# Performance work log

Hardware: AMD Instinct MI355X
Metric: run time of the kernel (lower is better)

The kernel has to match this reference:

```python
import jax, jax.numpy as jnp
import numpy as np

N_NODES = 100000
N_EDGES = 1600000
D_FEAT = 64


def setup_inputs() -> dict:
    key = jax.random.key(0)
    k1, k2, k3, k4 = jax.random.split(key, 4)
    rows = jax.random.randint(k1, (N_EDGES,), 0, N_NODES, dtype=jnp.int32)
    cols = jax.random.randint(k2, (N_EDGES,), 0, N_NODES, dtype=jnp.int32)
    vals = jax.random.uniform(k3, (N_EDGES,), dtype=jnp.float32)
    embeds = jax.random.normal(k4, (N_NODES, D_FEAT), dtype=jnp.float32)
    return {"rows": rows, "cols": cols, "vals": vals, "embeds": embeds,
            "n_nodes": N_NODES}


def reference(rows, cols, vals, embeds, n_nodes):
    # GCN sparse aggregation: res[i] = sum_{e: rows[e]==i} vals[e] * embeds[cols[e]]
    # Equivalent to adj.matmul(embeds) with adj in COO form.
    msgs = vals[:, None] * embeds[cols]            # [E, D] gather + scale
    res = jax.ops.segment_sum(msgs, rows, num_segments=n_nodes)  # [N, D] scatter-add
    return res
```

## Files before the change

kernel.cpp:

```cpp
#include <hip/hip_runtime.h>
#include <hip/hip_bf16.h>


#define D_FEAT 64
#define LOG_RPB 7
#define ROWS_PER_BUCKET 128
#define N_BUCKETS 782
#define PB 512
#define K1_CAP 3136
#define K4_CAP 3072

typedef unsigned long long u64;

__global__ __launch_bounds__(256) void gcn_scatter_fallback(
    const int* __restrict__ rows, const int* __restrict__ cols,
    const float* __restrict__ vals, const float* __restrict__ embeds,
    float* __restrict__ out, int n_edges)
{
    int gtid = blockIdx.x * blockDim.x + threadIdx.x;
    int e = gtid >> 4;
    if (e >= n_edges) return;
    int lane4 = gtid & 15;
    int row = rows[e]; int col = cols[e]; float v = vals[e];
    const float4* ep = reinterpret_cast<const float4*>(embeds + (size_t)col * D_FEAT);
    float4 m = ep[lane4];
    float* op = out + (size_t)row * D_FEAT + lane4 * 4;
    atomicAdd(op + 0, v * m.x);
    atomicAdd(op + 1, v * m.y);
    atomicAdd(op + 2, v * m.z);
    atomicAdd(op + 3, v * m.w);
}

__device__ inline int wave_incl_scan(int x, int lane) {
    #pragma unroll
    for (int o = 1; o < 64; o <<= 1) {
        int y = __shfl_up(x, o, 64);
        if (lane >= o) x += y;
    }
    return x;
}

__global__ __launch_bounds__(1024, 8) void k_partition_conv(
    const int* __restrict__ rows, const int* __restrict__ cols,
    const float* __restrict__ vals, u64* __restrict__ sorted,
    int* __restrict__ offg, const float* __restrict__ embeds,
    unsigned short* __restrict__ emb16, int do_conv,
    int n_edges, int n_elems, int chunk)
{
    __shared__ u64 ebuf[K1_CAP];
    __shared__ int lh[N_BUCKETS];
    __shared__ int cur[N_BUCKETS];
    __shared__ int segtot[16];

    int blk = blockIdx.x, tid = threadIdx.x;
    int lane = tid & 63, wid = tid >> 6;
    int beg = blk * chunk;
    int end = min(beg + chunk, n_edges);
    int cnt = end - beg;

    for (int i = tid; i < N_BUCKETS; i += 1024) lh[i] = 0;
    __syncthreads();
    for (int e = beg + tid; e < end; e += 1024)
        atomicAdd(&lh[rows[e] >> LOG_RPB], 1);
    __syncthreads();

    for (int seg = wid; seg * 64 < N_BUCKETS; seg += 16) {
        int idx = seg * 64 + lane;
        int v = (idx < N_BUCKETS) ? lh[idx] : 0;
        int inc = wave_incl_scan(v, lane);
        if (idx < N_BUCKETS) lh[idx] = inc - v;
        if (lane == 63) segtot[seg] = inc;
    }
    __syncthreads();
    if (tid < 64) {
        int v = (tid < 13) ? segtot[tid] : 0;
        int inc = wave_incl_scan(v, tid);
        if (tid < 13) segtot[tid] = inc - v;
    }
    __syncthreads();
    int* myoff = offg + (size_t)blk * (N_BUCKETS + 1);
    for (int i = tid; i < N_BUCKETS; i += 1024) {
        int excl = lh[i] + segtot[i >> 6];
        myoff[i] = excl;
        cur[i] = excl;
    }
    if (tid == 0) myoff[N_BUCKETS] = cnt;
    __syncthreads();

    for (int e = beg + tid; e < end; e += 1024) {
        int r = rows[e];
        int b = r >> LOG_RPB;
        unsigned meta = (unsigned)cols[e] |
                        ((unsigned)(r & (ROWS_PER_BUCKET - 1)) << 17);
        u64 ent = ((u64)__float_as_uint(vals[e]) << 32) | meta;
        int p = atomicAdd(&cur[b], 1);
        ebuf[p] = ent;
    }
    __syncthreads();

    for (int i = tid; i < cnt; i += 1024)
        sorted[beg + i] = ebuf[i];

    if (do_conv) {
        for (int i = blk * 1024 + tid; i < n_elems; i += PB * 1024) {
            unsigned u = __float_as_uint(embeds[i]);
            unsigned r = (u + 0x7FFFu + ((u >> 16) & 1u)) >> 16;
            emb16[i] = (unsigned short)r;
        }
    }
}

template <bool USE16>
__global__ __launch_bounds__(512) void k_aggregate_seg(
    const u64* __restrict__ sorted, const int* __restrict__ offg,
    const float* __restrict__ embeds, const unsigned short* __restrict__ emb16,
    float* __restrict__ out, int n_nodes, int chunk)
{
    __shared__ u64 ebuf[K4_CAP];
    __shared__ int sOff[PB], sLen[PB], sBase[PB];
    __shared__ int wtot[8];
    __shared__ int rcnt[ROWS_PER_BUCKET];
    __shared__ int roff[ROWS_PER_BUCKET + 1];
    __shared__ int rcur[ROWS_PER_BUCKET];

    int b = blockIdx.x, tid = threadIdx.x;
    int lane = tid & 63, wid = tid >> 6;
    int rowbase = b * ROWS_PER_BUCKET;
    int nrows = n_nodes - rowbase;
    if (nrows > ROWS_PER_BUCKET) nrows = ROWS_PER_BUCKET;

    if (tid < PB) {
        int o0 = offg[(size_t)tid * (N_BUCKETS + 1) + b];
        int o1 = offg[(size_t)tid * (N_BUCKETS + 1) + b + 1];
        sOff[tid] = o0;
        sLen[tid] = o1 - o0;
    }
    for (int i = tid; i < ROWS_PER_BUCKET; i += 512) rcnt[i] = 0;
    __syncthreads();

    {
        int v = sLen[wid * 64 + lane];
        int inc = wave_incl_scan(v, lane);
        sBase[wid * 64 + lane] = inc - v;
        if (lane == 63) wtot[wid] = inc;
    }
    __syncthreads();
    {
        int c = 0;
        for (int w = 0; w < wid; ++w) c += wtot[w];
        sBase[wid * 64 + lane] += c;
    }
    int n = 0;
    for (int w = 0; w < 8; ++w) n += wtot[w];
    __syncthreads();

    if (n <= K4_CAP) {
        for (int g = wid; g < PB / 16; g += 8) {
            int seg = g * 16 + (lane >> 2);
            int len = sLen[seg];
            const u64* sp = sorted + (size_t)seg * chunk + sOff[seg];
            for (int i = (lane & 3); i < len; i += 4)
                atomicAdd(&rcnt[(int)((sp[i] >> 17) & (ROWS_PER_BUCKET - 1))], 1);
        }
        __syncthreads();

        if (tid < 64) {
            int a = rcnt[tid], c = rcnt[64 + tid];
            int ia = wave_incl_scan(a, tid);
            int ta = __shfl(ia, 63, 64);
            int ic = wave_incl_scan(c, tid);
            int ea = ia - a;
            int ec = ta + ic - c;
            roff[tid] = ea;       rcur[tid] = ea;
            roff[64 + tid] = ec;  rcur[64 + tid] = ec;
            if (tid == 63) roff[ROWS_PER_BUCKET] = ta + __shfl(ic, 63, 64);
        }
        __syncthreads();

        for (int g = wid; g < PB / 16; g += 8) {
            int seg = g * 16 + (lane >> 2);
            int len = sLen[seg];
            const u64* sp = sorted + (size_t)seg * chunk + sOff[seg];
            for (int i = (lane & 3); i < len; i += 4) {
                u64 ent = sp[i];
                int lr = (int)((ent >> 17) & (ROWS_PER_BUCKET - 1));
                int p = atomicAdd(&rcur[lr], 1);
                ebuf[p] = ent;
            }
        }
        __syncthreads();

        for (int lr = wid; lr < ROWS_PER_BUCKET; lr += 8) {
            int rs = roff[lr], re = roff[lr + 1];
            float acc = 0.0f;
            int j = rs;
            #define GATHER(t) (USE16 \
                ? __uint_as_float((unsigned)emb16[(size_t)((t) & 0x1FFFF) * D_FEAT + lane] << 16) \
                : embeds[(size_t)((t) & 0x1FFFF) * D_FEAT + lane])
            for (; j + 7 < re; j += 8) {
                u64 t0 = ebuf[j + 0], t1 = ebuf[j + 1], t2 = ebuf[j + 2], t3 = ebuf[j + 3];
                u64 t4 = ebuf[j + 4], t5 = ebuf[j + 5], t6 = ebuf[j + 6], t7 = ebuf[j + 7];
                float m0 = GATHER(t0), m1 = GATHER(t1), m2 = GATHER(t2), m3 = GATHER(t3);
                float m4 = GATHER(t4), m5 = GATHER(t5), m6 = GATHER(t6), m7 = GATHER(t7);
                acc += __uint_as_float((unsigned)(t0 >> 32)) * m0;
                acc += __uint_as_float((unsigned)(t1 >> 32)) * m1;
                acc += __uint_as_float((unsigned)(t2 >> 32)) * m2;
                acc += __uint_as_float((unsigned)(t3 >> 32)) * m3;
                acc += __uint_as_float((unsigned)(t4 >> 32)) * m4;
                acc += __uint_as_float((unsigned)(t5 >> 32)) * m5;
                acc += __uint_as_float((unsigned)(t6 >> 32)) * m6;
                acc += __uint_as_float((unsigned)(t7 >> 32)) * m7;
            }
            for (; j + 3 < re; j += 4) {
                u64 t0 = ebuf[j + 0], t1 = ebuf[j + 1], t2 = ebuf[j + 2], t3 = ebuf[j + 3];
                float m0 = GATHER(t0), m1 = GATHER(t1), m2 = GATHER(t2), m3 = GATHER(t3);
                acc += __uint_as_float((unsigned)(t0 >> 32)) * m0;
                acc += __uint_as_float((unsigned)(t1 >> 32)) * m1;
                acc += __uint_as_float((unsigned)(t2 >> 32)) * m2;
                acc += __uint_as_float((unsigned)(t3 >> 32)) * m3;
            }
            for (; j < re; ++j) {
                u64 t0 = ebuf[j];
                acc += __uint_as_float((unsigned)(t0 >> 32)) * GATHER(t0);
            }
            #undef GATHER
            if (lr < nrows)
                out[(size_t)(rowbase + lr) * D_FEAT + lane] = acc;
        }
    } else {
        for (int i = tid; i < nrows * D_FEAT; i += 512)
            out[(size_t)rowbase * D_FEAT + i] = 0.0f;
        __syncthreads();
        for (int seg = wid; seg < PB; seg += 8) {
            int len = sLen[seg];
            const u64* sp = sorted + (size_t)seg * chunk + sOff[seg];
            for (int i = 0; i < len; ++i) {
                u64 ent = sp[i];
                int lr = (int)((ent >> 17) & (ROWS_PER_BUCKET - 1));
                int c = (int)(ent & 0x1FFFF);
                float v = __uint_as_float((unsigned)(ent >> 32));
                float m = embeds[(size_t)c * D_FEAT + lane];
                atomicAdd(&out[(size_t)(rowbase + lr) * D_FEAT + lane], v * m);
            }
        }
    }
}

extern "C" void kernel_launch(void* const* d_in, const int* in_sizes, int n_in,
                              void* d_out, int out_size, void* d_ws, size_t ws_size,
                              hipStream_t stream) {
    const int*   rows   = (const int*)d_in[0];
    const int*   cols   = (const int*)d_in[1];
    const float* vals   = (const float*)d_in[2];
    const float* embeds = (const float*)d_in[3];

    float* out = (float*)d_out;
    int n_edges = in_sizes[0];
    int n_nodes = out_size / D_FEAT;
    int n_buckets = (n_nodes + ROWS_PER_BUCKET - 1) >> LOG_RPB;
    int chunk = (n_edges + PB - 1) / PB;
    int n_elems = n_nodes * D_FEAT;

    size_t base_need = (size_t)n_edges * sizeof(u64) +
                       (size_t)PB * (N_BUCKETS + 1) * sizeof(int) + 256;
    size_t full_need = base_need + (size_t)n_elems * sizeof(unsigned short) + 256;

    if (n_buckets != N_BUCKETS || chunk > K1_CAP || ws_size < base_need) {
        hipMemsetAsync(out, 0, (size_t)out_size * sizeof(float), stream);
        long long total_threads = (long long)n_edges * 16;
        int block = 256;
        int grid = (int)((total_threads + block - 1) / block);
        gcn_scatter_fallback<<<grid, block, 0, stream>>>(rows, cols, vals, embeds, out, n_edges);
        return;
    }

    u64* sorted = (u64*)d_ws;
    int* offg   = (int*)(sorted + n_edges);
    unsigned short* emb16 = (unsigned short*)
        (((uintptr_t)(offg + (size_t)PB * (N_BUCKETS + 1)) + 15) & ~(uintptr_t)15);

    bool use16 = (ws_size >= full_need);

    k_partition_conv<<<PB, 1024, 0, stream>>>(rows, cols, vals, sorted, offg,
                                              embeds, emb16, use16 ? 1 : 0,
                                              n_edges, n_elems, chunk);
    if (use16)
        k_aggregate_seg<true><<<N_BUCKETS, 512, 0, stream>>>(
            sorted, offg, embeds, emb16, out, n_nodes, chunk);
    else
        k_aggregate_seg<false><<<N_BUCKETS, 512, 0, stream>>>(
            sorted, offg, embeds, emb16, out, n_nodes, chunk);
}
```

Baseline: 152.5 us.

## Fuse partition and aggregation into one cooperative kernel with a work queue

Merges the bucket-partition and per-bucket aggregation kernels into one cooperative launch of 512 blocks of 1024 threads, separated by grid.sync. After the sync, blocks pull buckets from a global atomic work queue. Edges are now loaded once into registers and reused for both the histogram and scatter passes, and the bf16 conversion is vectorised to float4. A global-atomic fallback is added for buckets whose edges exceed shared-memory capacity. The cooperative launch needs all 512 blocks to be co-resident, and the larger shared footprint plus 1024-thread blocks in the aggregation phase may lower occupancy and latency hiding for the gathers.

```diff
diff --git a/kernel.cpp b/kernel.cpp
--- a/kernel.cpp
+++ b/kernel.cpp
@@ -1,5 +1,8 @@
 #include <hip/hip_runtime.h>
 #include <hip/hip_bf16.h>
+#include <hip/hip_cooperative_groups.h>
+
+namespace cg = cooperative_groups;
 
 
 #define D_FEAT 64
@@ -8,9 +11,22 @@
 #define N_BUCKETS 782
 #define PB 512
 #define K1_CAP 3136
-#define K4_CAP 3072
 
 typedef unsigned long long u64;
+
+__device__ inline unsigned bf16rne(float x) {
+    unsigned u = __float_as_uint(x);
+    return (u + 0x7FFFu + ((u >> 16) & 1u)) >> 16;
+}
+
+__device__ inline int wave_incl_scan(int x, int lane) {
+    #pragma unroll
+    for (int o = 1; o < 64; o <<= 1) {
+        int y = __shfl_up(x, o, 64);
+        if (lane >= o) x += y;
+    }
+    return x;
+}
 
 __global__ __launch_bounds__(256) void gcn_scatter_fallback(
     const int* __restrict__ rows, const int* __restrict__ cols,
@@ -31,13 +47,231 @@
     atomicAdd(op + 3, v * m.w);
 }
 
-__device__ inline int wave_incl_scan(int x, int lane) {
-    #pragma unroll
-    for (int o = 1; o < 64; o <<= 1) {
-        int y = __shfl_up(x, o, 64);
-        if (lane >= o) x += y;
-    }
-    return x;
+template <bool USE16>
+__global__ __launch_bounds__(1024, 8) void k_fused(
+    const int* __restrict__ rows, const int* __restrict__ cols,
+    const float* __restrict__ vals, const float* __restrict__ embeds,
+    unsigned short* __restrict__ emb16, u64* __restrict__ sorted,
+    int* __restrict__ offg, int* __restrict__ wq, float* __restrict__ out,
+    int n_edges, int n_nodes, int n_elems, int chunk)
+{
+    __shared__ u64 ebuf[K1_CAP];
+    __shared__ int lh[N_BUCKETS];
+    __shared__ int cur[N_BUCKETS];
+    __shared__ int segtot[16];
+    __shared__ int sOff[PB], sLen[PB];
+    __shared__ int wtot[16];
+    __shared__ int rcnt[ROWS_PER_BUCKET];
+    __shared__ int roff[ROWS_PER_BUCKET + 1];
+    __shared__ int rcur[ROWS_PER_BUCKET];
+    __shared__ int sbucket;
+
+    cg::grid_group grid = cg::this_grid();
+
+    int blk = blockIdx.x, tid = threadIdx.x;
+    int lane = tid & 63, wid = tid >> 6;
+
+    {
+        int beg = blk * chunk;
+        int end = min(beg + chunk, n_edges);
+        int cnt = end - beg;
+
+        for (int i = tid; i < N_BUCKETS; i += 1024) lh[i] = 0;
+        __syncthreads();
+
+        u64 ent[4]; int eb[4]; bool okk[4];
+        #pragma unroll
+        for (int k = 0; k < 4; ++k) {
+            int e = beg + k * 1024 + tid;
+            okk[k] = (e < end);
+            if (okk[k]) {
+                int r = rows[e];
+                eb[k] = r >> LOG_RPB;
+                unsigned meta = (unsigned)cols[e] |
+                                ((unsigned)(r & (ROWS_PER_BUCKET - 1)) << 17);
+                ent[k] = ((u64)__float_as_uint(vals[e]) << 32) | meta;
+                atomicAdd(&lh[eb[k]], 1);
+            }
+        }
+        __syncthreads();
+
+        for (int seg = wid; seg * 64 < N_BUCKETS; seg += 16) {
+            int idx = seg * 64 + lane;
+            int v = (idx < N_BUCKETS) ? lh[idx] : 0;
+            int inc = wave_incl_scan(v, lane);
+            if (idx < N_BUCKETS) lh[idx] = inc - v;
+            if (lane == 63) segtot[seg] = inc;
+        }
+        __syncthreads();
+        if (tid < 64) {
+            int v = (tid < 13) ? segtot[tid] : 0;
+            int inc = wave_incl_scan(v, tid);
+            if (tid < 13) segtot[tid] = inc - v;
+        }
+        __syncthreads();
+        int* myoff = offg + (size_t)blk * (N_BUCKETS + 1);
+        for (int i = tid; i < N_BUCKETS; i += 1024) {
+            int excl = lh[i] + segtot[i >> 6];
+            myoff[i] = excl;
+            cur[i] = excl;
+        }
+        if (tid == 0) myoff[N_BUCKETS] = cnt;
+        __syncthreads();
+
+        #pragma unroll
+        for (int k = 0; k < 4; ++k) {
+            if (okk[k]) {
+                int p = atomicAdd(&cur[eb[k]], 1);
+                ebuf[p] = ent[k];
+            }
+        }
+        __syncthreads();
+
+        for (int i = tid; i < cnt; i += 1024)
+            sorted[beg + i] = ebuf[i];
+
+        if (USE16) {
+            const float4* src4 = (const float4*)embeds;
+            u64* dst4 = (u64*)emb16;
+            int nq = n_elems >> 2;
+            for (int i = blk * 1024 + tid; i < nq; i += PB * 1024) {
+                float4 f = src4[i];
+                u64 pk = (u64)bf16rne(f.x) | ((u64)bf16rne(f.y) << 16) |
+                         ((u64)bf16rne(f.z) << 32) | ((u64)bf16rne(f.w) << 48);
+                dst4[i] = pk;
+            }
+            if (blk == 0 && tid < (n_elems & 3)) {
+                int i = (nq << 2) + tid;
+                emb16[i] = (unsigned short)bf16rne(embeds[i]);
+            }
+        }
+        if (blk == 0 && tid == 0) *wq = 0;
+    }
+
+    grid.sync();
+
+    for (;;) {
+        __syncthreads();
+        if (tid == 0) sbucket = atomicAdd(wq, 1);
+        __syncthreads();
+        int b = sbucket;
+        if (b >= N_BUCKETS) break;
+
+        int rowbase = b * ROWS_PER_BUCKET;
+        int nrows = n_nodes - rowbase;
+        if (nrows > ROWS_PER_BUCKET) nrows = ROWS_PER_BUCKET;
+
+        if (tid < PB) {
+            int o0 = offg[(size_t)tid * (N_BUCKETS + 1) + b];
+            int o1 = offg[(size_t)tid * (N_BUCKETS + 1) + b + 1];
+            sOff[tid] = o0;
+            sLen[tid] = o1 - o0;
+        }
+        for (int i = tid; i < ROWS_PER_BUCKET; i += 1024) rcnt[i] = 0;
+        __syncthreads();
+
+        if (wid < 8) {
+            int v = sLen[wid * 64 + lane];
+            #pragma unroll
+            for (int o = 32; o > 0; o >>= 1) v += __shfl_down(v, o, 64);
+            if (lane == 0) wtot[wid] = v;
+        }
+        __syncthreads();
+        int n = 0;
+        #pragma unroll
+        for (int w = 0; w < 8; ++w) n += wtot[w];
+
+        if (n <= K1_CAP) {
+            {
+                int seg = tid >> 1;
+                int len = sLen[seg];
+                const u64* sp = sorted + (size_t)seg * chunk + sOff[seg];
+                for (int i = (tid & 1); i < len; i += 2)
+                    atomicAdd(&rcnt[(int)((sp[i] >> 17) & (ROWS_PER_BUCKET - 1))], 1);
+            }
+            __syncthreads();
+
+            if (tid < 64) {
+                int a = rcnt[tid], c = rcnt[64 + tid];
+                int ia = wave_incl_scan(a, tid);
+                int ta = __shfl(ia, 63, 64);
+                int ic = wave_incl_scan(c, tid);
+                int ea = ia - a;
+                int ec = ta + ic - c;
+                roff[tid] = ea;       rcur[tid] = ea;
+                roff[64 + tid] = ec;  rcur[64 + tid] = ec;
+                if (tid == 63) roff[ROWS_PER_BUCKET] = ta + __shfl(ic, 63, 64);
+            }
+            __syncthreads();
+
+            {
+                int seg = tid >> 1;
+                int len = sLen[seg];
+                const u64* sp = sorted + (size_t)seg * chunk + sOff[seg];
+                for (int i = (tid & 1); i < len; i += 2) {
+                    u64 ent = sp[i];
+                    int lr = (int)((ent >> 17) & (ROWS_PER_BUCKET - 1));
+                    int p = atomicAdd(&rcur[lr], 1);
+                    ebuf[p] = ent;
+                }
+            }
+            __syncthreads();
+
+            for (int lr = wid; lr < ROWS_PER_BUCKET; lr += 16) {
+                int rs = roff[lr], re = roff[lr + 1];
+                float acc = 0.0f;
+                int j = rs;
+                #define GATHER(t) (USE16 \
+                    ? __uint_as_float((unsigned)emb16[(size_t)((t) & 0x1FFFF) * D_FEAT + lane] << 16) \
+                    : embeds[(size_t)((t) & 0x1FFFF) * D_FEAT + lane])
+                for (; j + 7 < re; j += 8) {
+                    u64 t0 = ebuf[j + 0], t1 = ebuf[j + 1], t2 = ebuf[j + 2], t3 = ebuf[j + 3];
+                    u64 t4 = ebuf[j + 4], t5 = ebuf[j + 5], t6 = ebuf[j + 6], t7 = ebuf[j + 7];
+                    float m0 = GATHER(t0), m1 = GATHER(t1), m2 = GATHER(t2), m3 = GATHER(t3);
+                    float m4 = GATHER(t4), m5 = GATHER(t5), m6 = GATHER(t6), m7 = GATHER(t7);
+                    acc += __uint_as_float((unsigned)(t0 >> 32)) * m0;
+                    acc += __uint_as_float((unsigned)(t1 >> 32)) * m1;
+                    acc += __uint_as_float((unsigned)(t2 >> 32)) * m2;
+                    acc += __uint_as_float((unsigned)(t3 >> 32)) * m3;
+                    acc += __uint_as_float((unsigned)(t4 >> 32)) * m4;
+                    acc += __uint_as_float((unsigned)(t5 >> 32)) * m5;
+                    acc += __uint_as_float((unsigned)(t6 >> 32)) * m6;
+                    acc += __uint_as_float((unsigned)(t7 >> 32)) * m7;
+                }
+                for (; j + 3 < re; j += 4) {
+                    u64 t0 = ebuf[j + 0], t1 = ebuf[j + 1], t2 = ebuf[j + 2], t3 = ebuf[j + 3];
+                    float m0 = GATHER(t0), m1 = GATHER(t1), m2 = GATHER(t2), m3 = GATHER(t3);
+                    acc += __uint_as_float((unsigned)(t0 >> 32)) * m0;
+                    acc += __uint_as_float((unsigned)(t1 >> 32)) * m1;
+                    acc += __uint_as_float((unsigned)(t2 >> 32)) * m2;
+                    acc += __uint_as_float((unsigned)(t3 >> 32)) * m3;
+                }
+                for (; j < re; ++j) {
+                    u64 t0 = ebuf[j];
+                    acc += __uint_as_float((unsigned)(t0 >> 32)) * GATHER(t0);
+                }
+                #undef GATHER
+                if (lr < nrows)
+                    out[(size_t)(rowbase + lr) * D_FEAT + lane] = acc;
+            }
+        } else {
+            for (int i = tid; i < nrows * D_FEAT; i += 1024)
+                out[(size_t)rowbase * D_FEAT + i] = 0.0f;
+            __syncthreads();
+            for (int seg = wid; seg < PB; seg += 16) {
+                int len = sLen[seg];
+                const u64* sp = sorted + (size_t)seg * chunk + sOff[seg];
+                for (int i = 0; i < len; ++i) {
+                    u64 ent = sp[i];
+                    int lr = (int)((ent >> 17) & (ROWS_PER_BUCKET - 1));
+                    int c = (int)(ent & 0x1FFFF);
+                    float v = __uint_as_float((unsigned)(ent >> 32));
+                    float m = embeds[(size_t)c * D_FEAT + lane];
+                    atomicAdd(&out[(size_t)(rowbase + lr) * D_FEAT + lane], v * m);
+                }
+            }
+        }
+    }
 }
 
 __global__ __launch_bounds__(1024, 8) void k_partition_conv(
@@ -60,10 +294,21 @@
 
     for (int i = tid; i < N_BUCKETS; i += 1024) lh[i] = 0;
     __syncthreads();
-    for (int e = beg + tid; e < end; e += 1024)
-        atomicAdd(&lh[rows[e] >> LOG_RPB], 1);
-    __syncthreads();
-
+    u64 ent[4]; int eb[4]; bool okk[4];
+    #pragma unroll
+    for (int k = 0; k < 4; ++k) {
+        int e = beg + k * 1024 + tid;
+        okk[k] = (e < end);
+        if (okk[k]) {
+            int r = rows[e];
+            eb[k] = r >> LOG_RPB;
+            unsigned meta = (unsigned)cols[e] |
+                            ((unsigned)(r & (ROWS_PER_BUCKET - 1)) << 17);
+            ent[k] = ((u64)__float_as_uint(vals[e]) << 32) | meta;
+            atomicAdd(&lh[eb[k]], 1);
+        }
+    }
+    __syncthreads();
     for (int seg = wid; seg * 64 < N_BUCKETS; seg += 16) {
         int idx = seg * 64 + lane;
         int v = (idx < N_BUCKETS) ? lh[idx] : 0;
@@ -86,26 +331,20 @@
     }
     if (tid == 0) myoff[N_BUCKETS] = cnt;
     __syncthreads();
-
-    for (int e = beg + tid; e < end; e += 1024) {
-        int r = rows[e];
-        int b = r >> LOG_RPB;
-        unsigned meta = (unsigned)cols[e] |
-                        ((unsigned)(r & (ROWS_PER_BUCKET - 1)) << 17);
-        u64 ent = ((u64)__float_as_uint(vals[e]) << 32) | meta;
-        int p = atomicAdd(&cur[b], 1);
-        ebuf[p] = ent;
-    }
-    __syncthreads();
-
+    #pragma unroll
+    for (int k = 0; k < 4; ++k) {
+        if (okk[k]) {
+            int p = atomicAdd(&cur[eb[k]], 1);
+            ebuf[p] = ent[k];
+        }
+    }
+    __syncthreads();
     for (int i = tid; i < cnt; i += 1024)
         sorted[beg + i] = ebuf[i];
 
     if (do_conv) {
         for (int i = blk * 1024 + tid; i < n_elems; i += PB * 1024) {
-            unsigned u = __float_as_uint(embeds[i]);
-            unsigned r = (u + 0x7FFFu + ((u >> 16) & 1u)) >> 16;
-            emb16[i] = (unsigned short)r;
+            emb16[i] = (unsigned short)bf16rne(embeds[i]);
         }
     }
 }
@@ -116,8 +355,8 @@
     const float* __restrict__ embeds, const unsigned short* __restrict__ emb16,
     float* __restrict__ out, int n_nodes, int chunk)
 {
-    __shared__ u64 ebuf[K4_CAP];
-    __shared__ int sOff[PB], sLen[PB], sBase[PB];
+    __shared__ u64 ebuf[K1_CAP];
+    __shared__ int sOff[PB], sLen[PB];
     __shared__ int wtot[8];
     __shared__ int rcnt[ROWS_PER_BUCKET];
     __shared__ int roff[ROWS_PER_BUCKET + 1];
@@ -140,21 +379,16 @@
 
     {
         int v = sLen[wid * 64 + lane];
-        int inc = wave_incl_scan(v, lane);
-        sBase[wid * 64 + lane] = inc - v;
-        if (lane == 63) wtot[wid] = inc;
-    }
-    __syncthreads();
-    {
-        int c = 0;
-        for (int w = 0; w < wid; ++w) c += wtot[w];
-        sBase[wid * 64 + lane] += c;
-    }
+        #pragma unroll
+        for (int o = 32; o > 0; o >>= 1) v += __shfl_down(v, o, 64);
+        if (lane == 0) wtot[wid] = v;
+    }
+    __syncthreads();
     int n = 0;
+    #pragma unroll
     for (int w = 0; w < 8; ++w) n += wtot[w];
-    __syncthreads();
-
-    if (n <= K4_CAP) {
+
+    if (n <= K1_CAP) {
         for (int g = wid; g < PB / 16; g += 8) {
             int seg = g * 16 + (lane >> 2);
             int len = sLen[seg];
@@ -163,7 +397,6 @@
                 atomicAdd(&rcnt[(int)((sp[i] >> 17) & (ROWS_PER_BUCKET - 1))], 1);
         }
         __syncthreads();
-
         if (tid < 64) {
             int a = rcnt[tid], c = rcnt[64 + tid];
             int ia = wave_incl_scan(a, tid);
@@ -176,7 +409,6 @@
             if (tid == 63) roff[ROWS_PER_BUCKET] = ta + __shfl(ic, 63, 64);
         }
         __syncthreads();
-
         for (int g = wid; g < PB / 16; g += 8) {
             int seg = g * 16 + (lane >> 2);
             int len = sLen[seg];
@@ -189,7 +421,6 @@
             }
         }
         __syncthreads();
-
         for (int lr = wid; lr < ROWS_PER_BUCKET; lr += 8) {
             int rs = roff[lr], re = roff[lr + 1];
             float acc = 0.0f;
@@ -262,10 +493,11 @@
     int n_elems = n_nodes * D_FEAT;
 
     size_t base_need = (size_t)n_edges * sizeof(u64) +
-                       (size_t)PB * (N_BUCKETS + 1) * sizeof(int) + 256;
+                       ((size_t)PB * (N_BUCKETS + 1) + 1) * sizeof(int) + 256;
     size_t full_need = base_need + (size_t)n_elems * sizeof(unsigned short) + 256;
 
-    if (n_buckets != N_BUCKETS || chunk > K1_CAP || ws_size < base_need) {
+    if (n_buckets != N_BUCKETS || chunk > K1_CAP || chunk > 4096 ||
+        ws_size < base_need) {
         hipMemsetAsync(out, 0, (size_t)out_size * sizeof(float), stream);
         long long total_threads = (long long)n_edges * 16;
         int block = 256;
@@ -276,10 +508,31 @@
 
     u64* sorted = (u64*)d_ws;
     int* offg   = (int*)(sorted + n_edges);
+    int* wq     = offg + (size_t)PB * (N_BUCKETS + 1);
     unsigned short* emb16 = (unsigned short*)
-        (((uintptr_t)(offg + (size_t)PB * (N_BUCKETS + 1)) + 15) & ~(uintptr_t)15);
+        (((uintptr_t)(wq + 1) + 15) & ~(uintptr_t)15);
 
     bool use16 = (ws_size >= full_need);
+
+    int dev = 0, coop = 0;
+    hipGetDevice(&dev);
+    hipDeviceGetAttribute(&coop, hipDeviceAttributeCooperativeLaunch, dev);
+
+    if (coop) {
+        void* kargs[] = {
+            (void*)&rows, (void*)&cols, (void*)&vals, (void*)&embeds,
+            (void*)&emb16, (void*)&sorted, (void*)&offg, (void*)&wq,
+            (void*)&out, (void*)&n_edges, (void*)&n_nodes, (void*)&n_elems,
+            (void*)&chunk };
+        hipError_t err;
+        if (use16)
+            err = hipLaunchCooperativeKernel((const void*)k_fused<true>,
+                                             dim3(PB), dim3(1024), kargs, 0, stream);
+        else
+            err = hipLaunchCooperativeKernel((const void*)k_fused<false>,
+                                             dim3(PB), dim3(1024), kargs, 0, stream);
+        if (err == hipSuccess) return;
+    }
 
     k_partition_conv<<<PB, 1024, 0, stream>>>(rows, cols, vals, sorted, offg,
                                               embeds, emb16, use16 ? 1 : 0,
```

After: 242.4 us. 58.9% more time.

## Halve partition blocks, keep edges in registers, vectorize bf16 conversion

Applied to the files above, without the earlier changes.

Cuts the partition grid from 512 to 256 blocks with doubled chunk size, so the aggregate kernel reads half as many per-block segments and offset entries. Each thread loads its up to seven edges once into registers, which removes the second global read pass over rows/cols/vals. The bf16 embedding conversion now processes float4 loads into packed 64-bit stores. The aggregate kernel drops the unused per-segment scan in favour of a plain reduction and assigns two threads per segment. In exchange, the partition kernel uses more shared memory and registers per block and has fewer blocks to spread across the GPU.

```diff
diff --git a/kernel.cpp b/kernel.cpp
--- a/kernel.cpp
+++ b/kernel.cpp
@@ -6,11 +6,26 @@
 #define LOG_RPB 7
 #define ROWS_PER_BUCKET 128
 #define N_BUCKETS 782
-#define PB 512
-#define K1_CAP 3136
+#define PB 256
+#define K1_CAP 6272
+#define EPT 7
 #define K4_CAP 3072
 
 typedef unsigned long long u64;
+
+__device__ inline unsigned bf16rne(float x) {
+    unsigned u = __float_as_uint(x);
+    return (u + 0x7FFFu + ((u >> 16) & 1u)) >> 16;
+}
+
+__device__ inline int wave_incl_scan(int x, int lane) {
+    #pragma unroll
+    for (int o = 1; o < 64; o <<= 1) {
+        int y = __shfl_up(x, o, 64);
+        if (lane >= o) x += y;
+    }
+    return x;
+}
 
 __global__ __launch_bounds__(256) void gcn_scatter_fallback(
     const int* __restrict__ rows, const int* __restrict__ cols,
@@ -31,16 +46,7 @@
     atomicAdd(op + 3, v * m.w);
 }
 
-__device__ inline int wave_incl_scan(int x, int lane) {
-    #pragma unroll
-    for (int o = 1; o < 64; o <<= 1) {
-        int y = __shfl_up(x, o, 64);
-        if (lane >= o) x += y;
-    }
-    return x;
-}
-
-__global__ __launch_bounds__(1024, 8) void k_partition_conv(
+__global__ __launch_bounds__(1024, 4) void k_partition_conv(
     const int* __restrict__ rows, const int* __restrict__ cols,
     const float* __restrict__ vals, u64* __restrict__ sorted,
     int* __restrict__ offg, const float* __restrict__ embeds,
@@ -60,8 +66,21 @@
 
     for (int i = tid; i < N_BUCKETS; i += 1024) lh[i] = 0;
     __syncthreads();
-    for (int e = beg + tid; e < end; e += 1024)
-        atomicAdd(&lh[rows[e] >> LOG_RPB], 1);
+
+    u64 ent[EPT]; int eb[EPT]; bool okk[EPT];
+    #pragma unroll
+    for (int k = 0; k < EPT; ++k) {
+        int e = beg + k * 1024 + tid;
+        okk[k] = (e < end);
+        if (okk[k]) {
+            int r = rows[e];
+            eb[k] = r >> LOG_RPB;
+            unsigned meta = (unsigned)cols[e] |
+                            ((unsigned)(r & (ROWS_PER_BUCKET - 1)) << 17);
+            ent[k] = ((u64)__float_as_uint(vals[e]) << 32) | meta;
+            atomicAdd(&lh[eb[k]], 1);
+        }
+    }
     __syncthreads();
 
     for (int seg = wid; seg * 64 < N_BUCKETS; seg += 16) {
@@ -87,14 +106,12 @@
     if (tid == 0) myoff[N_BUCKETS] = cnt;
     __syncthreads();
 
-    for (int e = beg + tid; e < end; e += 1024) {
-        int r = rows[e];
-        int b = r >> LOG_RPB;
-        unsigned meta = (unsigned)cols[e] |
-                        ((unsigned)(r & (ROWS_PER_BUCKET - 1)) << 17);
-        u64 ent = ((u64)__float_as_uint(vals[e]) << 32) | meta;
-        int p = atomicAdd(&cur[b], 1);
-        ebuf[p] = ent;
+    #pragma unroll
+    for (int k = 0; k < EPT; ++k) {
+        if (okk[k]) {
+            int p = atomicAdd(&cur[eb[k]], 1);
+            ebuf[p] = ent[k];
+        }
     }
     __syncthreads();
 
@@ -102,10 +119,18 @@
         sorted[beg + i] = ebuf[i];
 
     if (do_conv) {
-        for (int i = blk * 1024 + tid; i < n_elems; i += PB * 1024) {
-            unsigned u = __float_as_uint(embeds[i]);
-            unsigned r = (u + 0x7FFFu + ((u >> 16) & 1u)) >> 16;
-            emb16[i] = (unsigned short)r;
+        const float4* src4 = (const float4*)embeds;
+        u64* dst4 = (u64*)emb16;
+        int nq = n_elems >> 2;
+        for (int i = blk * 1024 + tid; i < nq; i += PB * 1024) {
+            float4 f = src4[i];
+            u64 pk = (u64)bf16rne(f.x) | ((u64)bf16rne(f.y) << 16) |
+                     ((u64)bf16rne(f.z) << 32) | ((u64)bf16rne(f.w) << 48);
+            dst4[i] = pk;
+        }
+        if (blk == 0 && tid < (n_elems & 3)) {
+            int i = (nq << 2) + tid;
+            emb16[i] = (unsigned short)bf16rne(embeds[i]);
         }
     }
 }
@@ -117,8 +142,8 @@
     float* __restrict__ out, int n_nodes, int chunk)
 {
     __shared__ u64 ebuf[K4_CAP];
-    __shared__ int sOff[PB], sLen[PB], sBase[PB];
-    __shared__ int wtot[8];
+    __shared__ int sOff[PB], sLen[PB];
+    __shared__ int wtot[4];
     __shared__ int rcnt[ROWS_PER_BUCKET];
     __shared__ int roff[ROWS_PER_BUCKET + 1];
     __shared__ int rcur[ROWS_PER_BUCKET];
@@ -138,28 +163,21 @@
     for (int i = tid; i < ROWS_PER_BUCKET; i += 512) rcnt[i] = 0;
     __syncthreads();
 
-    {
+    if (wid < 4) {
         int v = sLen[wid * 64 + lane];
-        int inc = wave_incl_scan(v, lane);
-        sBase[wid * 64 + lane] = inc - v;
-        if (lane == 63) wtot[wid] = inc;
-    }
-    __syncthreads();
-    {
-        int c = 0;
-        for (int w = 0; w < wid; ++w) c += wtot[w];
-        sBase[wid * 64 + lane] += c;
-    }
-    int n = 0;
-    for (int w = 0; w < 8; ++w) n += wtot[w];
-    __syncthreads();
+        #pragma unroll
+        for (int o = 32; o > 0; o >>= 1) v += __shfl_down(v, o, 64);
+        if (lane == 0) wtot[wid] = v;
+    }
+    __syncthreads();
+    int n = wtot[0] + wtot[1] + wtot[2] + wtot[3];
 
     if (n <= K4_CAP) {
-        for (int g = wid; g < PB / 16; g += 8) {
-            int seg = g * 16 + (lane >> 2);
+        {
+            int seg = tid >> 1;
             int len = sLen[seg];
             const u64* sp = sorted + (size_t)seg * chunk + sOff[seg];
-            for (int i = (lane & 3); i < len; i += 4)
+            for (int i = (tid & 1); i < len; i += 2)
                 atomicAdd(&rcnt[(int)((sp[i] >> 17) & (ROWS_PER_BUCKET - 1))], 1);
         }
         __syncthreads();
@@ -177,11 +195,11 @@
         }
         __syncthreads();
 
-        for (int g = wid; g < PB / 16; g += 8) {
-            int seg = g * 16 + (lane >> 2);
+        {
+            int seg = tid >> 1;
             int len = sLen[seg];
             const u64* sp = sorted + (size_t)seg * chunk + sOff[seg];
-            for (int i = (lane & 3); i < len; i += 4) {
+            for (int i = (tid & 1); i < len; i += 2) {
                 u64 ent = sp[i];
                 int lr = (int)((ent >> 17) & (ROWS_PER_BUCKET - 1));
                 int p = atomicAdd(&rcur[lr], 1);
@@ -265,7 +283,8 @@
                        (size_t)PB * (N_BUCKETS + 1) * sizeof(int) + 256;
     size_t full_need = base_need + (size_t)n_elems * sizeof(unsigned short) + 256;
 
-    if (n_buckets != N_BUCKETS || chunk > K1_CAP || ws_size < base_need) {
+    if (n_buckets != N_BUCKETS || chunk > K1_CAP || chunk > EPT * 1024 ||
+        ws_size < base_need) {
         hipMemsetAsync(out, 0, (size_t)out_size * sizeof(float), stream);
         long long total_threads = (long long)n_edges * 16;
         int block = 256;
```

Result: no change. 150.6 us (-1.3%).
